# Kernel optimization log

Hardware: AMD Instinct MI355X
Metric: run time of the kernel (lower is better)

Reference implementation:

```python
import jax, jax.numpy as jnp
import numpy as np

WS = 3          # windows_size
ND = 3          # num_dilation, dilations [1,2,3]
NSTATE = 16     # d_state
RANK = 12       # dt_rank = ceil(192/16)
TOPK = 36       # max(1,(20//3)**2)*depth
DM = 192        # d_model
DI = 384        # d_inner = 2*d_model
B0, HH, WW = 8, 96, 96


def setup_inputs() -> dict:
    ks = jax.random.split(jax.random.key(0), 12)
    f = jax.random.normal
    return {
        "x": f(ks[0], (B0, HH, WW, DM), jnp.float32),
        "W_in": f(ks[1], (2 * DI, DM), jnp.float32) * 0.02,
        "conv_w": f(ks[2], (DI, 1, 7, 7), jnp.float32) * 0.05,
        "conv_b": f(ks[3], (DI,), jnp.float32) * 0.01,
        "x_proj_w": f(ks[4], (2, RANK + 2 * NSTATE, DI), jnp.float32) * 0.02,
        "dt_w": f(ks[5], (2, DI, RANK), jnp.float32) * 0.02,
        "dt_b": f(ks[6], (2, DI), jnp.float32) * 0.01,
        "A_logs": jnp.tile(jnp.log(jnp.arange(1, NSTATE + 1, dtype=jnp.float32)), (2 * DI, 1)),
        "Ds": jnp.ones((2 * DI,), jnp.float32),
        "W_kv": f(ks[7], (2 * DI, DI), jnp.float32) * 0.02,
        "b_kv": jnp.zeros((2 * DI,), jnp.float32),
        "ln_g": jnp.ones((DI,), jnp.float32),
        "ln_b": jnp.zeros((DI,), jnp.float32),
        "W_out": f(ks[8], (DM, DI), jnp.float32) * 0.02,
    }


def _selective_scan(xs, x_proj_w, dt_w, dt_b, A_logs, Ds):
    # xs: (B, K=2, D, L) -> (B, K, D, L). Standard Mamba selective scan.
    B, K, D, L = xs.shape
    x_dbl = jnp.einsum('bkdl,kcd->bkcl', xs, x_proj_w)          # (B,K,R+2N,L)
    dts = x_dbl[:, :, :RANK]
    Bs = x_dbl[:, :, RANK:RANK + NSTATE]                        # (B,K,N,L)
    Cs = x_dbl[:, :, RANK + NSTATE:]                            # (B,K,N,L)
    delta = jax.nn.softplus(jnp.einsum('bkrl,kdr->bkdl', dts, dt_w) + dt_b[None, :, :, None])
    A = -jnp.exp(A_logs).reshape(K, D, NSTATE)
    dA = jnp.exp(delta[..., None] * A[None, :, :, None, :])    # (B,K,D,L,N)
    dBu = delta[..., None] * Bs.transpose(0, 1, 3, 2)[:, :, None, :, :] * xs[..., None]
    dA = jnp.moveaxis(dA, 3, 0)                                 # (L,B,K,D,N)
    dBu = jnp.moveaxis(dBu, 3, 0)
    C = jnp.moveaxis(Cs, 3, 0)                                  # (L,B,K,N)

    def step(h, inp):
        dA_t, dBu_t, C_t = inp
        h = dA_t * h + dBu_t
        y = jnp.einsum('bkdn,bkn->bkd', h, C_t)
        return h, y

    h0 = jnp.zeros((B, K, D, NSTATE), xs.dtype)
    _, ys = jax.lax.scan(step, h0, (dA, dBu, C))                # ys: (L,B,K,D)
    y = jnp.moveaxis(ys, 0, 3)                                  # (B,K,D,L)
    return y + Ds.reshape(1, K, D, 1) * xs


def _dynamic_mask_active(x):
    # x: (B,D,H,W). Partition into WSxWS windows, keep TOPK by mean activation.
    B, D, H, W = x.shape
    nH, nW = H // WS, W // WS
    w = x.reshape(B, D, nH, WS, nW, WS).transpose(0, 2, 4, 1, 3, 5)
    w = w.reshape(B, nH * nW, D, WS * WS)                       # (B,nWin,D,ws2)
    score = w.mean(axis=(2, 3))                                 # (B,nWin)
    _, idx = jax.lax.top_k(score, TOPK)                         # (B,TOPK)
    g = jnp.take_along_axis(w, idx[:, :, None, None], axis=1)   # (B,TOPK,D,ws2)
    return g.transpose(0, 2, 1, 3).reshape(B, D, TOPK * WS * WS)


def _unfold(x, d):
    # torch nn.Unfold(kernel=WS, dilation=d, padding=d, stride=1) on (B,C,H,W)
    B, C, H, W = x.shape
    xp = jnp.pad(x, ((0, 0), (0, 0), (d, d), (d, d)))
    pats = [xp[:, :, i * d:i * d + H, j * d:j * d + W] for i in range(WS) for j in range(WS)]
    p = jnp.stack(pats, axis=2)                                 # (B,C,ws2,H,W) channel-major like torch
    return p.reshape(B, C, WS * WS, H * W)


def _forward(x, W_in, conv_w, conv_b, x_proj_w, dt_w, dt_b, A_logs, Ds,
             W_kv, b_kv, ln_g, ln_b, W_out):
    B, H, W_, _ = x.shape
    xz = jnp.einsum('bhwc,oc->bhwo', x, W_in)
    xf, z = jnp.split(xz, 2, axis=-1)                           # (B,H,W,DI) each
    xc = xf.transpose(0, 3, 1, 2)
    xc = jax.lax.conv_general_dilated(xc, conv_w, (1, 1), [(3, 3), (3, 3)],
                                      feature_group_count=conv_w.shape[0],
                                      dimension_numbers=('NCHW', 'OIHW', 'NCHW'))
    xc = xc + conv_b[None, :, None, None]                       # (B,DI,H,W)
    D = xc.shape[1]

    # foreground SSM on active windows (forward + flipped scan)
    act = _dynamic_mask_active(xc)                              # (B,D,L)
    xs = jnp.stack([act, jnp.flip(act, axis=-1)], axis=1)       # (B,2,D,L)
    out = _selective_scan(xs, x_proj_w, dt_w, dt_b, A_logs, Ds)
    y1 = out[:, 0] + jnp.flip(out[:, 1], axis=-1)               # (B,D,L)
    y1 = y1.transpose(0, 2, 1)                                  # (B,L,D)

    L = y1.shape[1]
    ws2 = WS * WS
    n2 = L // ws2
    kv = jnp.einsum('bld,od->blo', y1, W_kv) + b_kv             # (B,L,2D)
    hd = 2 * D // ND
    t = kv.reshape(B, n2, ws2, ND, hd).transpose(3, 0, 4, 2, 1)  # (ND,B,hd,ws2,n2)
    Q, Kt = t[:, :, :hd // 2], t[:, :, hd // 2:]                 # (ND,B,D/ND,ws2,n2)

    dch = D // ND
    xr = xc.reshape(B, ND, dch, H, W_)
    ys = []
    for i in range(ND):
        V = _unfold(xr[:, i], i + 1)                            # (B,dch,ws2,n1)
        V = V.transpose(0, 1, 3, 2)                             # (B,dch,n1,ws2)
        s = jnp.einsum('bcwn,bcwn->bcw', Q[i], Kt[i]) / np.sqrt(dch).astype(np.float32)
        # softmax over a singleton axis (as in the source) -> all ones
        A_M = jax.nn.softmax(s[..., None], axis=-1)[..., 0]     # (B,dch,ws2)
        ys.append(jnp.einsum('bcnw,bcw->bcn', V, A_M))          # (B,dch,n1)
    y = jnp.concatenate(ys, axis=1)                             # (B,D,n1)
    y = y.transpose(0, 2, 1)                                    # (B,n1,D)

    mu = y.mean(-1, keepdims=True)
    var = y.var(-1, keepdims=True)
    y = (y - mu) / jnp.sqrt(var + 1e-5) * ln_g + ln_b
    y = y.reshape(B, H, W_, D) + z
    return jnp.einsum('bhwd,od->bhwo', y, W_out)


def reference(x, W_in, conv_w, conv_b, x_proj_w, dt_w, dt_b, A_logs, Ds,
              W_kv, b_kv, ln_g, ln_b, W_out):
    return _forward(x, W_in, conv_w, conv_b, x_proj_w, dt_w, dt_b, A_logs, Ds,
                    W_kv, b_kv, ln_g, ln_b, W_out)
```

## Files before the change

### kernel.cpp

```cpp
#include <hip/hip_runtime.h>
#include <cstddef>

#define B0V 8
#define HSV 96
#define WSV 96
#define DMV 192
#define DIV 384
#define MTOT (B0V*HSV*WSV)

typedef __attribute__((ext_vector_type(8))) unsigned short ushort8v;
typedef __attribute__((ext_vector_type(8))) short short8v;
typedef __attribute__((ext_vector_type(4))) float f32x4;
typedef _Float16 h2 __attribute__((ext_vector_type(2)));
typedef _Float16 h8 __attribute__((ext_vector_type(8)));

__device__ __forceinline__ unsigned short f2bf(float f) {
    unsigned int i; __builtin_memcpy(&i, &f, 4);
    i += 0x7FFFu + ((i >> 16) & 1);
    return (unsigned short)(i >> 16);
}

template<int ROWS>
__device__ __forceinline__ void stageBF16(const unsigned short* __restrict__ src, int ld,
                                          unsigned short* lds, int t) {
#pragma unroll
    for (int i = 0; i < ROWS*8/256; ++i) {
        const int cid = t + i*256;
        const int r = cid >> 3, cb = cid & 7;
        ushort8v sv = *(const ushort8v*)(src + (size_t)r*ld + cb*8);
        *(ushort8v*)((char*)lds + r*128 + ((cb ^ (r&7))<<4)) = sv;
    }
}
__device__ __forceinline__ short8v fragRead(const unsigned short* lds, int row, int kchunk) {
    return *(const short8v*)((const char*)lds + row*128 + ((kchunk ^ (row&7))<<4));
}

__global__ __launch_bounds__(192) void wc_kernel(
    const float* __restrict__ Wout, const float* __restrict__ Win,
    unsigned short* __restrict__ Wch)
{
    const int o = blockIdx.x;
    const int c = threadIdx.x;
    __shared__ float wrow[384];
    for (int j = threadIdx.x; j < 384; j += 192) wrow[j] = Wout[(size_t)o*384 + j];
    __syncthreads();
    float acc = 0.f;
#pragma unroll 4
    for (int j = 0; j < 384; ++j)
        acc += wrow[j] * Win[(size_t)(384 + j)*192 + c];
    Wch[(size_t)o*192 + c] = f2bf(acc);
}

__global__ __launch_bounds__(256) void wprep_kernel(
    const float* __restrict__ cw, h2* __restrict__ w2h)
{
    const int idx = blockIdx.x*256 + threadIdx.x;
    if (idx < 49*192) {
        const int tap = idx / 192, cp = idx % 192;
        h2 v;
        v[0] = (_Float16)cw[(size_t)(2*cp  )*49 + tap];
        v[1] = (_Float16)cw[(size_t)(2*cp+1)*49 + tap];
        w2h[idx] = v;
    }
}

__global__ __launch_bounds__(256) void cvt_kernel(
    const float* __restrict__ src, unsigned short* __restrict__ dst, int n8)
{
    const int i = blockIdx.x*256 + threadIdx.x;
    if (i < n8) {
        const float4 f0 = *(const float4*)(src + (size_t)i*8);
        const float4 f1 = *(const float4*)(src + (size_t)i*8 + 4);
        ushort8v v;
        v[0]=f2bf(f0.x); v[1]=f2bf(f0.y); v[2]=f2bf(f0.z); v[3]=f2bf(f0.w);
        v[4]=f2bf(f1.x); v[5]=f2bf(f1.y); v[6]=f2bf(f1.z); v[7]=f2bf(f1.w);
        *(ushort8v*)(dst + (size_t)i*8) = v;
    }
}

__global__ __launch_bounds__(256) void gemm_in_mfma(
    const float* __restrict__ x, const unsigned short* __restrict__ Wh,
    unsigned short* __restrict__ xh, _Float16* __restrict__ xf)
{
    __shared__ unsigned short As[3*128*64];
    __shared__ unsigned short Bs[128*64];
    const int t = threadIdx.x;
    const int m0 = blockIdx.x * 128;
    const int wid = t >> 6, lane = t & 63;
    const int wm = wid >> 1, wn = wid & 1;
    const int li = lane & 15, lg = lane >> 4;

#pragma unroll
    for (int kb = 0; kb < 3; ++kb) {
#pragma unroll
        for (int i = 0; i < 4; ++i) {
            const int cid = t + i*256;
            const int r = cid >> 3, cb = cid & 7;
            const float* p = x + (size_t)(m0 + r)*DMV + kb*64 + cb*8;
            float4 f0 = *(const float4*)p;
            float4 f1 = *(const float4*)(p+4);
            ushort8v sv;
            sv[0]=f2bf(f0.x); sv[1]=f2bf(f0.y); sv[2]=f2bf(f0.z); sv[3]=f2bf(f0.w);
            sv[4]=f2bf(f1.x); sv[5]=f2bf(f1.y); sv[6]=f2bf(f1.z); sv[7]=f2bf(f1.w);
            *(ushort8v*)((char*)(As + kb*128*64) + r*128 + ((cb ^ (r&7))<<4)) = sv;
            *(ushort8v*)(xh + (size_t)(m0 + r)*DMV + kb*64 + cb*8) = sv;
        }
    }

    for (int n0i = 0; n0i < 3; ++n0i) {
        const int n0 = n0i * 128;
        f32x4 acc[4][4];
#pragma unroll
        for (int i = 0; i < 4; ++i)
#pragma unroll
            for (int j = 0; j < 4; ++j) acc[i][j] = (f32x4){0.f,0.f,0.f,0.f};

        for (int kb = 0; kb < 3; ++kb) {
            __syncthreads();
            stageBF16<128>(Wh + (size_t)n0*DMV + kb*64, DMV, Bs, t);
            __syncthreads();
#pragma unroll
            for (int ks = 0; ks < 2; ++ks) {
                short8v a[4], b[4];
#pragma unroll
                for (int mf = 0; mf < 4; ++mf)
                    a[mf] = fragRead(As + kb*128*64, wm*64 + mf*16 + li, ks*4 + lg);
#pragma unroll
                for (int nf = 0; nf < 4; ++nf)
                    b[nf] = fragRead(Bs, wn*64 + nf*16 + li, ks*4 + lg);
#pragma unroll
                for (int mf = 0; mf < 4; ++mf)
#pragma unroll
                    for (int nf = 0; nf < 4; ++nf)
                        acc[mf][nf] = __builtin_amdgcn_mfma_f32_16x16x32_bf16(a[mf], b[nf], acc[mf][nf], 0, 0, 0);
            }
        }
#pragma unroll
        for (int mf = 0; mf < 4; ++mf)
#pragma unroll
            for (int nf = 0; nf < 4; ++nf)
#pragma unroll
                for (int i = 0; i < 4; ++i) {
                    const int row = m0 + wm*64 + mf*16 + lg*4 + i;
                    const int col = n0 + wn*64 + nf*16 + li;
                    xf[(size_t)row*DIV + col] = (_Float16)acc[mf][nf][i];
                }
    }
}

__global__ __launch_bounds__(256) void dwconv_kernel(
    const _Float16* __restrict__ xf, const h2* __restrict__ w2h,
    const float* __restrict__ cb, _Float16* __restrict__ xc)
{
    const int tile = blockIdx.x;
    const int th = tile / 3, tw = tile % 3;
    const int h0 = th*8, w0 = tw*32;
    const int c0 = blockIdx.y*64, b = blockIdx.z;

    __shared__ _Float16 patch[14*38*64];
    const int t = threadIdx.x;
    for (int idx = t; idx < 14*38*8; idx += 256) {
        const int sp = idx >> 3, c8 = idx & 7;
        const int ih = sp / 38, iw = sp - ih*38;
        const int gh = h0 - 3 + ih, gw = w0 - 3 + iw;
        ushort8v v;
#pragma unroll
        for (int j = 0; j < 8; ++j) v[j] = 0;
        if ((unsigned)gh < (unsigned)HSV && (unsigned)gw < (unsigned)WSV)
            v = *(const ushort8v*)(xf + (((size_t)b*HSV + gh)*WSV + gw)*DIV + c0 + c8*8);
        *(ushort8v*)(patch + sp*64 + c8*8) = v;
    }
    __syncthreads();

    const int cp = t & 31;
    const int wq = t >> 5;

    h2 wreg[49];
    const h2* wp = w2h + (c0 >> 1) + cp;
#pragma unroll
    for (int k = 0; k < 49; ++k) wreg[k] = wp[k*192];

    h2 biasv;
    biasv[0] = (_Float16)cb[c0 + 2*cp];
    biasv[1] = (_Float16)cb[c0 + 2*cp + 1];
    h2 acc[8][4];
#pragma unroll
    for (int i = 0; i < 8; ++i)
#pragma unroll
        for (int j = 0; j < 4; ++j) acc[i][j] = biasv;

    const h2* prow = (const h2*)patch + wq*4*32 + cp;
#pragma unroll
    for (int ih = 0; ih < 14; ++ih) {
        h2 r[10];
#pragma unroll
        for (int jj = 0; jj < 10; ++jj)
            r[jj] = prow[(ih*38 + jj)*32];
#pragma unroll
        for (int kh = 0; kh < 7; ++kh) {
            const int oh = ih - kh;
            if (oh >= 0 && oh < 8) {
#pragma unroll
                for (int kw = 0; kw < 7; ++kw)
#pragma unroll
                    for (int j = 0; j < 4; ++j)
                        acc[oh][j] += wreg[kh*7 + kw] * r[j + kw];
            }
        }
    }
    h2* xcp = (h2*)xc;
#pragma unroll
    for (int oh = 0; oh < 8; ++oh)
#pragma unroll
        for (int j = 0; j < 4; ++j)
            xcp[((((size_t)b*HSV + h0+oh)*WSV + (w0 + wq*4 + j))*DIV + c0)/2 + cp] = acc[oh][j];
}

__global__ __launch_bounds__(256) void boxln_kernel(
    const _Float16* __restrict__ xc,
    const float* __restrict__ g, const float* __restrict__ bta,
    unsigned short* __restrict__ yln)
{
    const int wid  = threadIdx.x >> 6;
    const int lane = threadIdx.x & 63;
    const int m = blockIdx.x * 4 + wid;
    const int b  = m / (HSV*WSV);
    const int hw = m % (HSV*WSV);
    const int h = hw / WSV, w = hw % WSV;

    const bool act = lane < 48;
    const int ch = lane * 8;
    const int dd = (ch >> 7) + 1;

    float s[8];
#pragma unroll
    for (int j = 0; j < 8; ++j) s[j] = 0.f;

#pragma unroll
    for (int a = -1; a <= 1; ++a)
#pragma unroll
        for (int bb = -1; bb <= 1; ++bb) {
            const int h2_ = h + a*dd, w2_ = w + bb*dd;
            if (act && (unsigned)h2_ < (unsigned)HSV && (unsigned)w2_ < (unsigned)WSV) {
                h8 v = *(const h8*)(xc + (((size_t)b*HSV + h2_)*WSV + w2_)*DIV + ch);
#pragma unroll
                for (int j = 0; j < 8; ++j) s[j] += (float)v[j];
            }
        }

    float ps = 0.f, ps2 = 0.f;
#pragma unroll
    for (int j = 0; j < 8; ++j) { ps += s[j]; ps2 += s[j]*s[j]; }
#pragma unroll
    for (int off = 32; off > 0; off >>= 1) {
        ps  += __shfl_xor(ps,  off);
        ps2 += __shfl_xor(ps2, off);
    }
    const float mu   = ps * (1.f/384.f);
    const float var  = ps2 * (1.f/384.f) - mu*mu;
    const float rstd = rsqrtf(var + 1e-5f);

    if (act) {
        float4 g0 = *(const float4*)(g + ch);
        float4 g1 = *(const float4*)(g + ch + 4);
        float4 b0 = *(const float4*)(bta + ch);
        float4 b1 = *(const float4*)(bta + ch + 4);
        float gv[8] = {g0.x,g0.y,g0.z,g0.w,g1.x,g1.y,g1.z,g1.w};
        float bv[8] = {b0.x,b0.y,b0.z,b0.w,b1.x,b1.y,b1.z,b1.w};
        ushort8v o;
#pragma unroll
        for (int j = 0; j < 8; ++j)
            o[j] = f2bf((s[j] - mu)*rstd*gv[j] + bv[j]);
        *(ushort8v*)(yln + (size_t)m*DIV + ch) = o;
    }
}

__global__ __launch_bounds__(256) void gemm_out_mfma(
    const unsigned short* __restrict__ Yl, const unsigned short* __restrict__ WoutH,
    const unsigned short* __restrict__ xh, const unsigned short* __restrict__ Wch,
    float* __restrict__ out)
{
    __shared__ unsigned short As[128*64];
    __shared__ unsigned short Bs[192*64];
    const int t = threadIdx.x;
    const int m0 = blockIdx.x * 128;
    const int wid = t >> 6, lane = t & 63;
    const int wm = wid >> 1, wn = wid & 1;
    const int li = lane & 15, lg = lane >> 4;

    f32x4 acc[4][6];
#pragma unroll
    for (int i = 0; i < 4; ++i)
#pragma unroll
        for (int j = 0; j < 6; ++j) acc[i][j] = (f32x4){0.f,0.f,0.f,0.f};

    for (int kb = 0; kb < 9; ++kb) {
        if (kb < 6) {
            stageBF16<128>(Yl + (size_t)m0*DIV + kb*64, DIV, As, t);
            stageBF16<192>(WoutH + kb*64, DIV, Bs, t);
        } else {
            stageBF16<128>(xh + (size_t)m0*DMV + (kb-6)*64, DMV, As, t);
            stageBF16<192>(Wch + (kb-6)*64, DMV, Bs, t);
        }
        __syncthreads();
#pragma unroll
        for (int ks = 0; ks < 2; ++ks) {
            short8v a[4], b[6];
#pragma unroll
            for (int mf = 0; mf < 4; ++mf) a[mf] = fragRead(As, wm*64 + mf*16 + li, ks*4 + lg);
#pragma unroll
            for (int nf = 0; nf < 6; ++nf) b[nf] = fragRead(Bs, wn*96 + nf*16 + li, ks*4 + lg);
#pragma unroll
            for (int mf = 0; mf < 4; ++mf)
#pragma unroll
                for (int nf = 0; nf < 6; ++nf)
                    acc[mf][nf] = __builtin_amdgcn_mfma_f32_16x16x32_bf16(a[mf], b[nf], acc[mf][nf], 0, 0, 0);
        }
        __syncthreads();
    }
#pragma unroll
    for (int mf = 0; mf < 4; ++mf)
#pragma unroll
        for (int nf = 0; nf < 6; ++nf)
#pragma unroll
            for (int i = 0; i < 4; ++i) {
                const int row = m0 + wm*64 + mf*16 + lg*4 + i;
                const int col = wn*96 + nf*16 + li;
                out[(size_t)row*DMV + col] = acc[mf][nf][i];
            }
}

extern "C" void kernel_launch(void* const* d_in, const int* in_sizes, int n_in,
                              void* d_out, int out_size, void* d_ws, size_t ws_size,
                              hipStream_t stream)
{
    const float* x      = (const float*)d_in[0];
    const float* W_in   = (const float*)d_in[1];
    const float* conv_w = (const float*)d_in[2];
    const float* conv_b = (const float*)d_in[3];
    const float* ln_g   = (const float*)d_in[11];
    const float* ln_b   = (const float*)d_in[12];
    const float* W_out  = (const float*)d_in[13];
    float* out = (float*)d_out;

    char* ws = (char*)d_ws;
    unsigned short* Wch   = (unsigned short*)(ws);
    h2*             w2h   = (h2*)(ws + 0x20000);
    unsigned short* WinfH = (unsigned short*)(ws + 0x40000);
    unsigned short* WoutH = (unsigned short*)(ws + 0x80000);
    unsigned short* xh    = (unsigned short*)(ws + 0x100000);
    _Float16*       xf    = (_Float16*)(ws + 0x2000000);
    _Float16*       xc    = (_Float16*)d_out;

    wc_kernel    <<<dim3(192),          192, 0, stream>>>(W_out, W_in, Wch);
    wprep_kernel <<<dim3(37),           256, 0, stream>>>(conv_w, w2h);
    cvt_kernel   <<<dim3(36),           256, 0, stream>>>(W_in,  WinfH, 384*192/8);
    cvt_kernel   <<<dim3(36),           256, 0, stream>>>(W_out, WoutH, 192*384/8);
    gemm_in_mfma <<<dim3(MTOT/128),     256, 0, stream>>>(x, WinfH, xh, xf);
    dwconv_kernel<<<dim3(36, 6, B0V),   256, 0, stream>>>(xf, w2h, conv_b, xc);
    boxln_kernel <<<dim3(MTOT/4),       256, 0, stream>>>(xc, ln_g, ln_b,
                                                          (unsigned short*)xf);
    gemm_out_mfma<<<dim3(MTOT/128),     256, 0, stream>>>((const unsigned short*)xf,
                                                          WoutH, xh, Wch, out);
}
```

Measured before the change: 216.4 us.

## Shrink dwconv tiles, swizzle LDS patch, and accumulate box sums in half2

```diff
diff --git a/kernel.cpp b/kernel.cpp
--- a/kernel.cpp
+++ b/kernel.cpp
@@ -153,22 +153,22 @@
     const float* __restrict__ cb, _Float16* __restrict__ xc)
 {
     const int tile = blockIdx.x;
-    const int th = tile / 3, tw = tile % 3;
-    const int h0 = th*8, w0 = tw*32;
+    const int th = tile / 6, tw = tile % 6;
+    const int h0 = th*8, w0 = tw*16;
     const int c0 = blockIdx.y*64, b = blockIdx.z;
 
-    __shared__ _Float16 patch[14*38*64];
+    __shared__ _Float16 patch[14*22*64];
     const int t = threadIdx.x;
-    for (int idx = t; idx < 14*38*8; idx += 256) {
+    for (int idx = t; idx < 308*8; idx += 256) {
         const int sp = idx >> 3, c8 = idx & 7;
-        const int ih = sp / 38, iw = sp - ih*38;
+        const int ih = sp / 22, iw = sp - ih*22;
         const int gh = h0 - 3 + ih, gw = w0 - 3 + iw;
         ushort8v v;
 #pragma unroll
         for (int j = 0; j < 8; ++j) v[j] = 0;
         if ((unsigned)gh < (unsigned)HSV && (unsigned)gw < (unsigned)WSV)
             v = *(const ushort8v*)(xf + (((size_t)b*HSV + gh)*WSV + gw)*DIV + c0 + c8*8);
-        *(ushort8v*)(patch + sp*64 + c8*8) = v;
+        *(ushort8v*)((char*)patch + sp*128 + ((c8*16) ^ ((sp & 7) << 4))) = v;
     }
     __syncthreads();
 
@@ -183,28 +183,27 @@
     h2 biasv;
     biasv[0] = (_Float16)cb[c0 + 2*cp];
     biasv[1] = (_Float16)cb[c0 + 2*cp + 1];
-    h2 acc[8][4];
-#pragma unroll
-    for (int i = 0; i < 8; ++i)
-#pragma unroll
-        for (int j = 0; j < 4; ++j) acc[i][j] = biasv;
-
-    const h2* prow = (const h2*)patch + wq*4*32 + cp;
+    h2 acc[8][2];
+#pragma unroll
+    for (int i = 0; i < 8; ++i) { acc[i][0] = biasv; acc[i][1] = biasv; }
+
 #pragma unroll
     for (int ih = 0; ih < 14; ++ih) {
-        h2 r[10];
-#pragma unroll
-        for (int jj = 0; jj < 10; ++jj)
-            r[jj] = prow[(ih*38 + jj)*32];
+        h2 r[8];
+#pragma unroll
+        for (int j = 0; j < 8; ++j) {
+            const int sp = ih*22 + wq*2 + j;
+            r[j] = *(const h2*)((const char*)patch + sp*128 + ((cp*4) ^ ((sp & 7) << 4)));
+        }
 #pragma unroll
         for (int kh = 0; kh < 7; ++kh) {
             const int oh = ih - kh;
             if (oh >= 0 && oh < 8) {
 #pragma unroll
-                for (int kw = 0; kw < 7; ++kw)
-#pragma unroll
-                    for (int j = 0; j < 4; ++j)
-                        acc[oh][j] += wreg[kh*7 + kw] * r[j + kw];
+                for (int kw = 0; kw < 7; ++kw) {
+                    acc[oh][0] += wreg[kh*7 + kw] * r[kw];
+                    acc[oh][1] += wreg[kh*7 + kw] * r[kw + 1];
+                }
             }
         }
     }
@@ -212,8 +211,8 @@
 #pragma unroll
     for (int oh = 0; oh < 8; ++oh)
 #pragma unroll
-        for (int j = 0; j < 4; ++j)
-            xcp[((((size_t)b*HSV + h0+oh)*WSV + (w0 + wq*4 + j))*DIV + c0)/2 + cp] = acc[oh][j];
+        for (int j = 0; j < 2; ++j)
+            xcp[((((size_t)b*HSV + h0+oh)*WSV + (w0 + wq*2 + j))*DIV + c0)/2 + cp] = acc[oh][j];
 }
 
 __global__ __launch_bounds__(256) void boxln_kernel(
@@ -232,9 +231,9 @@
     const int ch = lane * 8;
     const int dd = (ch >> 7) + 1;
 
-    float s[8];
-#pragma unroll
-    for (int j = 0; j < 8; ++j) s[j] = 0.f;
+    h2 s2[4];
+#pragma unroll
+    for (int k = 0; k < 4; ++k) { s2[k][0] = (_Float16)0; s2[k][1] = (_Float16)0; }
 
 #pragma unroll
     for (int a = -1; a <= 1; ++a)
@@ -244,9 +243,16 @@
             if (act && (unsigned)h2_ < (unsigned)HSV && (unsigned)w2_ < (unsigned)WSV) {
                 h8 v = *(const h8*)(xc + (((size_t)b*HSV + h2_)*WSV + w2_)*DIV + ch);
 #pragma unroll
-                for (int j = 0; j < 8; ++j) s[j] += (float)v[j];
+                for (int k = 0; k < 4; ++k) {
+                    h2 p; p[0] = v[2*k]; p[1] = v[2*k+1];
+                    s2[k] += p;
+                }
             }
         }
+
+    float s[8];
+#pragma unroll
+    for (int k = 0; k < 4; ++k) { s[2*k] = (float)s2[k][0]; s[2*k+1] = (float)s2[k][1]; }
 
     float ps = 0.f, ps2 = 0.f;
 #pragma unroll
@@ -357,7 +363,7 @@
     cvt_kernel   <<<dim3(36),           256, 0, stream>>>(W_in,  WinfH, 384*192/8);
     cvt_kernel   <<<dim3(36),           256, 0, stream>>>(W_out, WoutH, 192*384/8);
     gemm_in_mfma <<<dim3(MTOT/128),     256, 0, stream>>>(x, WinfH, xh, xf);
-    dwconv_kernel<<<dim3(36, 6, B0V),   256, 0, stream>>>(xf, w2h, conv_b, xc);
+    dwconv_kernel<<<dim3(72, 6, B0V),   256, 0, stream>>>(xf, w2h, conv_b, xc);
     boxln_kernel <<<dim3(MTOT/4),       256, 0, stream>>>(xc, ln_g, ln_b,
                                                           (unsigned short*)xf);
     gemm_out_mfma<<<dim3(MTOT/128),     256, 0, stream>>>((const unsigned short*)xf,
```

Result: slower. 230.9 us (+6.7%).
